# Kernel tuning notes

Measured on AMD Instinct MI355X. Metric: run time of the kernel, lower is better.

The kernel has to match this reference:

```python
import jax, jax.numpy as jnp
import numpy as np

N, E, V_IN, HID, U_IN, B, MEM = 50000, 800000, 128, 128, 64, 64, 128
CAT = V_IN + HID + U_IN  # 320 == hidden*2 + u_in
ALPHA = 0.5
EPS = 1e-5


def setup_inputs() -> dict:
    key = jax.random.key(0)
    ks = jax.random.split(key, 12)
    x = jax.random.normal(ks[0], (N, V_IN), dtype=jnp.float32)
    edge_index = jax.random.randint(ks[1], (2, E), 0, N, dtype=jnp.int64)
    edge_attr = jax.random.normal(ks[2], (E, HID), dtype=jnp.float32)
    u = jax.random.normal(ks[3], (B, U_IN), dtype=jnp.float32)
    batch = jnp.sort(jax.random.randint(ks[4], (N,), 0, B, dtype=jnp.int64))
    Mk = jax.random.normal(ks[5], (MEM, CAT), dtype=jnp.float32)
    Mv = jax.random.normal(ks[6], (MEM, CAT), dtype=jnp.float32)
    ln_gamma = jnp.ones((CAT,), dtype=jnp.float32)
    ln_beta = jnp.zeros((CAT,), dtype=jnp.float32)
    W1 = jax.random.normal(ks[7], (CAT, HID), dtype=jnp.float32) * (1.0 / np.sqrt(CAT))
    b1 = jnp.zeros((HID,), dtype=jnp.float32)
    W2 = jax.random.normal(ks[8], (HID, HID), dtype=jnp.float32) * (1.0 / np.sqrt(HID))
    b2 = jnp.zeros((HID,), dtype=jnp.float32)
    return {"x": x, "edge_index": edge_index, "edge_attr": edge_attr, "u": u,
            "batch": batch, "Mk": Mk, "Mv": Mv, "ln_gamma": ln_gamma,
            "ln_beta": ln_beta, "W1": W1, "b1": b1, "W2": W2, "b2": b2}


def reference(x, edge_index, edge_attr, u, batch, Mk, Mv, ln_gamma, ln_beta, W1, b1, W2, b2):
    # scatter_add over destination nodes
    agg = jax.ops.segment_sum(edge_attr, edge_index[1], num_segments=N)  # [N, HID]
    out = jnp.concatenate([x, agg, u[batch]], axis=1)  # [N, CAT]
    # LayerNorm over last dim
    mu = jnp.mean(out, axis=-1, keepdims=True)
    var = jnp.var(out, axis=-1, keepdims=True)
    out = (out - mu) * jax.lax.rsqrt(var + EPS) * ln_gamma + ln_beta
    # External attention: [N,CAT] @ [CAT,MEM] -> softmax over MEM -> @ [MEM,CAT]
    scores = jnp.einsum('nc,mc->nm', out, Mk)
    attn = jax.nn.softmax(scores, axis=-1)
    attn_out = jnp.einsum('nm,mc->nc', attn, Mv)
    out = ALPHA * attn_out + (1.0 - ALPHA) * out
    # MLP
    h = jax.nn.relu(out @ W1 + b1)
    return h @ W2 + b2
```

## Files before the change

### kernel.cpp

```cpp
#include <hip/hip_runtime.h>

#define NN   50000
#define EE   800000
#define VIN  128
#define HIDN 128
#define UIN  64
#define MEMN 128
#define CATN 320
#define LN_EPS 1e-5f
#define SCAN_NB 196

typedef __attribute__((ext_vector_type(8))) short short8;
typedef __attribute__((ext_vector_type(4))) float f32x4;
typedef __attribute__((ext_vector_type(4))) unsigned int uint4v;
typedef __attribute__((ext_vector_type(4))) unsigned short ushort4v;
typedef unsigned short ushort_t;

__device__ inline ushort_t f32_bf16(float f) {
    unsigned u = __float_as_uint(f);
    return (ushort_t)((u + 0x7FFFu + ((u >> 16) & 1u)) >> 16);
}
__device__ inline float bf16_f32(ushort_t h) {
    return __uint_as_float(((unsigned)h) << 16);
}
__device__ inline unsigned pack_hl(float y) {
    unsigned u  = __float_as_uint(y);
    unsigned hi = (u + 0x7FFFu + ((u >> 16) & 1u)) & 0xFFFF0000u;
    float    lo = y - __uint_as_float(hi);
    unsigned v  = __float_as_uint(lo);
    unsigned l16 = ((v + 0x7FFFu + ((v >> 16) & 1u)) >> 16) & 0xFFFFu;
    return hi | l16;
}

__global__ void hist_kernel(const int* __restrict__ edge_dst, int* __restrict__ count)
{
    int gid = blockIdx.x * 256 + threadIdx.x;
    if (gid < EE) atomicAdd(&count[edge_dst[gid]], 1);
}

__global__ void block_sum_kernel(const int* __restrict__ count, int* __restrict__ partials)
{
    __shared__ int s[256];
    const int tid = threadIdx.x;
    const int gid = blockIdx.x * 256 + tid;
    s[tid] = (gid < NN) ? count[gid] : 0;
    __syncthreads();
    for (int off = 128; off >= 1; off >>= 1) {
        if (tid < off) s[tid] += s[tid + off];
        __syncthreads();
    }
    if (tid == 0) partials[blockIdx.x] = s[0];
}

__global__ void scan_partials_kernel(int* __restrict__ partials)
{
    __shared__ int s[256];
    const int tid = threadIdx.x;
    const int v = (tid < SCAN_NB) ? partials[tid] : 0;
    s[tid] = v;
    __syncthreads();
    for (int off = 1; off < 256; off <<= 1) {
        int t = (tid >= off) ? s[tid - off] : 0;
        __syncthreads();
        s[tid] += t;
        __syncthreads();
    }
    if (tid < SCAN_NB) partials[tid] = s[tid] - v;
}

__global__ void make_offsets_kernel(const int* __restrict__ count,
                                    const int* __restrict__ partials,
                                    int* __restrict__ offsets)
{
    __shared__ int s[256];
    const int tid = threadIdx.x;
    const int gid = blockIdx.x * 256 + tid;
    const int v = (gid < NN) ? count[gid] : 0;
    s[tid] = v;
    __syncthreads();
    for (int off = 1; off < 256; off <<= 1) {
        int t = (tid >= off) ? s[tid - off] : 0;
        __syncthreads();
        s[tid] += t;
        __syncthreads();
    }
    if (gid < NN) offsets[gid] = partials[blockIdx.x] + s[tid] - v;
}

__global__ void fill_kernel(const int* __restrict__ edge_dst,
                            const int* __restrict__ offsets,
                            int* __restrict__ cursor,
                            int* __restrict__ bucket)
{
    int gid = blockIdx.x * 256 + threadIdx.x;
    if (gid >= EE) return;
    const int d = edge_dst[gid];
    const int p = atomicAdd(&cursor[d], 1);
    bucket[offsets[d] + p] = gid;
}

__global__ void prep_all_kernel(const float* __restrict__ Mk,
                                const float* __restrict__ Mv,
                                const float* __restrict__ W1,
                                const float* __restrict__ W2,
                                ushort_t* __restrict__ mk_hi,
                                ushort_t* __restrict__ mk_lo,
                                ushort_t* __restrict__ mv_t,
                                ushort_t* __restrict__ w1_t,
                                ushort_t* __restrict__ w2_t)
{
    int i = blockIdx.x * 256 + threadIdx.x;
    if (i < MEMN * CATN) {
        const float f = Mk[i];
        const ushort_t h = f32_bf16(f);
        mk_hi[i] = h;
        mk_lo[i] = f32_bf16(f - bf16_f32(h));
    }
    if (i < CATN * MEMN) {
        const int c = i >> 7, m = i & 127;
        mv_t[i] = f32_bf16(Mv[m * CATN + c]);
    }
    if (i < HIDN * CATN) {
        const int n = i / CATN, k = i - n * CATN;
        w1_t[i] = f32_bf16(W1[k * HIDN + n]);
    }
    if (i < HIDN * HIDN) {
        const int n = i >> 7, k = i & 127;
        w2_t[i] = f32_bf16(W2[k * HIDN + n]);
    }
}

__global__ __launch_bounds__(256) void gather_ln_kernel(
    const float* __restrict__ edge_attr,
    const int*   __restrict__ bucket,
    const int*   __restrict__ offsets,
    const int*   __restrict__ count,
    const float* __restrict__ x,
    const float* __restrict__ u,
    const int*   __restrict__ batch,
    const float* __restrict__ gamma,
    const float* __restrict__ beta,
    unsigned*    __restrict__ ln_pk)
{
    const int wid  = (blockIdx.x * 256 + threadIdx.x) >> 6;
    const int lane = threadIdx.x & 63;
    if (wid >= NN) return;

    const int start = offsets[wid];
    const int deg   = count[wid];
    const float2* ea2 = reinterpret_cast<const float2*>(edge_attr);
    float2 a = make_float2(0.f, 0.f);
    int i = 0;
    const int d4 = deg & ~3;
    for (; i < d4; i += 4) {
        const int e0 = bucket[start + i];
        const int e1 = bucket[start + i + 1];
        const int e2 = bucket[start + i + 2];
        const int e3 = bucket[start + i + 3];
        const float2 v0 = ea2[(size_t)e0 * 64 + lane];
        const float2 v1 = ea2[(size_t)e1 * 64 + lane];
        const float2 v2 = ea2[(size_t)e2 * 64 + lane];
        const float2 v3 = ea2[(size_t)e3 * 64 + lane];
        a.x += (v0.x + v1.x) + (v2.x + v3.x);
        a.y += (v0.y + v1.y) + (v2.y + v3.y);
    }
    for (; i < deg; ++i) {
        const int e = bucket[start + i];
        const float2 v = ea2[(size_t)e * 64 + lane];
        a.x += v.x;
        a.y += v.y;
    }
    const float2 xv = reinterpret_cast<const float2*>(x)[(size_t)wid * 64 + lane];
    const float  uv = u[batch[wid] * UIN + lane];

    float s = xv.x + xv.y + a.x + a.y + uv;
    float q = xv.x * xv.x + xv.y * xv.y + a.x * a.x + a.y * a.y + uv * uv;
    #pragma unroll
    for (int off = 32; off >= 1; off >>= 1) {
        s += __shfl_xor(s, off);
        q += __shfl_xor(q, off);
    }
    const float mu  = s * (1.0f / CATN);
    const float var = q * (1.0f / CATN) - mu * mu;
    const float rs  = rsqrtf(var + LN_EPS);

    const float2 g0 = reinterpret_cast<const float2*>(gamma)[lane];
    const float2 g1 = reinterpret_cast<const float2*>(gamma)[64 + lane];
    const float  g2 = gamma[256 + lane];
    const float2 t0 = reinterpret_cast<const float2*>(beta)[lane];
    const float2 t1 = reinterpret_cast<const float2*>(beta)[64 + lane];
    const float  t2 = beta[256 + lane];

    unsigned* row = ln_pk + (size_t)wid * CATN;
    uint2 p01, p23;
    p01.x = pack_hl((xv.x - mu) * rs * g0.x + t0.x);
    p01.y = pack_hl((xv.y - mu) * rs * g0.y + t0.y);
    p23.x = pack_hl((a.x - mu) * rs * g1.x + t1.x);
    p23.y = pack_hl((a.y - mu) * rs * g1.y + t1.y);
    reinterpret_cast<uint2*>(row)[lane]       = p01;
    reinterpret_cast<uint2*>(row + 128)[lane] = p23;
    row[256 + lane] = pack_hl((uv - mu) * rs * g2 + t2);
}

#define MSTR 328
#define PSTR 136

__global__ __launch_bounds__(512) void node_mfma_kernel(
    const unsigned* __restrict__ ln_pk,
    const ushort_t* __restrict__ mk_hi,
    const ushort_t* __restrict__ mk_lo,
    const ushort_t* __restrict__ mv_t,
    const ushort_t* __restrict__ w1_t,
    const ushort_t* __restrict__ w2_t,
    const float*    __restrict__ b1,
    const float*    __restrict__ b2,
    float*          __restrict__ out)
{
    __shared__ __align__(16) ushort_t s_lnh[32 * MSTR];
    __shared__ __align__(16) ushort_t s_lnl[32 * MSTR];
    __shared__ __align__(16) ushort_t s_P[32 * PSTR];
    __shared__ __align__(16) float2   s_part[16 * 16];

    const int tid  = threadIdx.x;
    const int wv   = tid >> 6;
    const int lane = tid & 63;
    const int l15  = lane & 15;
    const int l4   = lane >> 4;
    const int node0 = blockIdx.x * 32;

    const f32x4 zero4 = {0.f, 0.f, 0.f, 0.f};

    for (int j = tid; j < 32 * 80; j += 512) {
        const int nl = j / 80;
        const int c0 = (j - nl * 80) * 4;
        int ng = node0 + nl; ng = (ng < NN) ? ng : (NN - 1);
        const uint4v p = *(const uint4v*)(ln_pk + (size_t)ng * CATN + c0);
        ushort4v h4, l4v;
        h4.x = (ushort_t)(p.x >> 16);  l4v.x = (ushort_t)(p.x & 0xFFFFu);
        h4.y = (ushort_t)(p.y >> 16);  l4v.y = (ushort_t)(p.y & 0xFFFFu);
        h4.z = (ushort_t)(p.z >> 16);  l4v.z = (ushort_t)(p.z & 0xFFFFu);
        h4.w = (ushort_t)(p.w >> 16);  l4v.w = (ushort_t)(p.w & 0xFFFFu);
        *(ushort4v*)(s_lnh + nl * MSTR + c0) = h4;
        *(ushort4v*)(s_lnl + nl * MSTR + c0) = l4v;
    }
    __syncthreads();

    {
        f32x4 acc[2];
        acc[0] = zero4; acc[1] = zero4;

        #pragma unroll 2
        for (int kc = 0; kc < 10; ++kc) {
            const int koff = kc * 32 + l4 * 8;
            const int mr = wv * 16 + l15;
            short8 amh = *(const short8*)(mk_hi + (size_t)mr * CATN + koff);
            short8 aml = *(const short8*)(mk_lo + (size_t)mr * CATN + koff);
            short8 bnh[2], bnl[2];
            #pragma unroll
            for (int bt = 0; bt < 2; ++bt) {
                bnh[bt] = *(const short8*)(s_lnh + (bt * 16 + l15) * MSTR + koff);
                bnl[bt] = *(const short8*)(s_lnl + (bt * 16 + l15) * MSTR + koff);
            }
            #pragma unroll
            for (int bt = 0; bt < 2; ++bt) {
                acc[bt] = __builtin_amdgcn_mfma_f32_16x16x32_bf16(amh, bnh[bt], acc[bt], 0, 0, 0);
                acc[bt] = __builtin_amdgcn_mfma_f32_16x16x32_bf16(aml, bnh[bt], acc[bt], 0, 0, 0);
                acc[bt] = __builtin_amdgcn_mfma_f32_16x16x32_bf16(amh, bnl[bt], acc[bt], 0, 0, 0);
            }
        }

        #pragma unroll
        for (int bt = 0; bt < 2; ++bt) {
            float mx = acc[bt][0];
            #pragma unroll
            for (int r = 1; r < 4; ++r) mx = fmaxf(mx, acc[bt][r]);
            mx = fmaxf(mx, __shfl_xor(mx, 16));
            mx = fmaxf(mx, __shfl_xor(mx, 32));
            float sm = 0.f;
            #pragma unroll
            for (int r = 0; r < 4; ++r) sm += __expf(acc[bt][r] - mx);
            sm += __shfl_xor(sm, 16);
            sm += __shfl_xor(sm, 32);
            if (l4 == 0) s_part[(wv * 2 + bt) * 16 + l15] = make_float2(mx, sm);
        }
        __syncthreads();
        #pragma unroll
        for (int bt = 0; bt < 2; ++bt) {
            float mg = -1e30f;
            float2 pw[8];
            #pragma unroll
            for (int w = 0; w < 8; ++w) {
                pw[w] = s_part[(w * 2 + bt) * 16 + l15];
                mg = fmaxf(mg, pw[w].x);
            }
            float sg = 0.f;
            #pragma unroll
            for (int w = 0; w < 8; ++w) sg += pw[w].y * __expf(pw[w].x - mg);
            const float inv = 1.f / sg;
            ushort_t* prow = s_P + (bt * 16 + l15) * PSTR + wv * 16 + l4 * 4;
            #pragma unroll
            for (int r = 0; r < 4; ++r)
                prow[r] = f32_bf16(__expf(acc[bt][r] - mg) * inv);
        }
    }
    __syncthreads();

    {
        const int mt = wv & 1;
        const int cg = wv >> 1;
        f32x4 acc[5];
        #pragma unroll
        for (int nn = 0; nn < 5; ++nn) acc[nn] = zero4;

        #pragma unroll
        for (int kc = 0; kc < 4; ++kc) {
            const int koff = kc * 32 + l4 * 8;
            short8 ap = *(const short8*)(s_P + (mt * 16 + l15) * PSTR + koff);
            short8 bv[5];
            #pragma unroll
            for (int nn = 0; nn < 5; ++nn) {
                const int c = (cg * 5 + nn) * 16 + l15;
                bv[nn] = *(const short8*)(mv_t + (size_t)c * MEMN + koff);
            }
            #pragma unroll
            for (int nn = 0; nn < 5; ++nn)
                acc[nn] = __builtin_amdgcn_mfma_f32_16x16x32_bf16(ap, bv[nn], acc[nn], 0, 0, 0);
        }
        __syncthreads();
        #pragma unroll
        for (int nn = 0; nn < 5; ++nn)
            #pragma unroll
            for (int r = 0; r < 4; ++r) {
                const int node_l = mt * 16 + l4 * 4 + r;
                const int c = (cg * 5 + nn) * 16 + l15;
                const int idx = node_l * MSTR + c;
                const float lnv = bf16_f32(s_lnh[idx]) + bf16_f32(s_lnl[idx]);
                s_lnh[idx] = f32_bf16(0.5f * (acc[nn][r] + lnv));
            }
    }
    __syncthreads();

    {
        const int mt  = wv & 1;
        const int ng2 = wv >> 1;
        f32x4 acc[2];
        acc[0] = zero4; acc[1] = zero4;

        #pragma unroll 2
        for (int kc = 0; kc < 10; ++kc) {
            const int koff = kc * 32 + l4 * 8;
            short8 am = *(const short8*)(s_lnh + (mt * 16 + l15) * MSTR + koff);
            short8 bw[2];
            #pragma unroll
            for (int nt = 0; nt < 2; ++nt) {
                const int n = (ng2 * 2 + nt) * 16 + l15;
                bw[nt] = *(const short8*)(w1_t + (size_t)n * CATN + koff);
            }
            #pragma unroll
            for (int nt = 0; nt < 2; ++nt)
                acc[nt] = __builtin_amdgcn_mfma_f32_16x16x32_bf16(am, bw[nt], acc[nt], 0, 0, 0);
        }
        float bb[2];
        #pragma unroll
        for (int nt = 0; nt < 2; ++nt) bb[nt] = b1[(ng2 * 2 + nt) * 16 + l15];
        __syncthreads();
        #pragma unroll
        for (int nt = 0; nt < 2; ++nt)
            #pragma unroll
            for (int r = 0; r < 4; ++r) {
                const int node_l = mt * 16 + l4 * 4 + r;
                const int col = (ng2 * 2 + nt) * 16 + l15;
                s_P[node_l * PSTR + col] = f32_bf16(fmaxf(acc[nt][r] + bb[nt], 0.f));
            }
    }
    __syncthreads();

    {
        const int mt  = wv & 1;
        const int ng2 = wv >> 1;
        f32x4 acc[2];
        acc[0] = zero4; acc[1] = zero4;

        #pragma unroll
        for (int kc = 0; kc < 4; ++kc) {
            const int koff = kc * 32 + l4 * 8;
            short8 ah = *(const short8*)(s_P + (mt * 16 + l15) * PSTR + koff);
            short8 bw[2];
            #pragma unroll
            for (int nt = 0; nt < 2; ++nt) {
                const int n = (ng2 * 2 + nt) * 16 + l15;
                bw[nt] = *(const short8*)(w2_t + (size_t)n * HIDN + koff);
            }
            #pragma unroll
            for (int nt = 0; nt < 2; ++nt)
                acc[nt] = __builtin_amdgcn_mfma_f32_16x16x32_bf16(ah, bw[nt], acc[nt], 0, 0, 0);
        }
        float bb[2];
        #pragma unroll
        for (int nt = 0; nt < 2; ++nt) bb[nt] = b2[(ng2 * 2 + nt) * 16 + l15];
        #pragma unroll
        for (int nt = 0; nt < 2; ++nt)
            #pragma unroll
            for (int r = 0; r < 4; ++r) {
                const int ng = node0 + (wv & 1) * 16 + l4 * 4 + r;
                if (ng < NN) {
                    const int col = (ng2 * 2 + nt) * 16 + l15;
                    out[(size_t)ng * HIDN + col] = acc[nt][r] + bb[nt];
                }
            }
    }
}

extern "C" void kernel_launch(void* const* d_in, const int* in_sizes, int n_in,
                              void* d_out, int out_size, void* d_ws, size_t ws_size,
                              hipStream_t stream)
{
    const float* x         = (const float*)d_in[0];
    const int*   edge_idx  = (const int*)  d_in[1];
    const float* edge_attr = (const float*)d_in[2];
    const float* u         = (const float*)d_in[3];
    const int*   batch     = (const int*)  d_in[4];
    const float* Mk        = (const float*)d_in[5];
    const float* Mv        = (const float*)d_in[6];
    const float* gamma     = (const float*)d_in[7];
    const float* beta      = (const float*)d_in[8];
    const float* W1        = (const float*)d_in[9];
    const float* b1        = (const float*)d_in[10];
    const float* W2        = (const float*)d_in[11];
    const float* b2        = (const float*)d_in[12];
    float*       out       = (float*)d_out;

    char* w = (char*)d_ws;
    int*   count     = (int*)w;        w += (size_t)NN * sizeof(int);
    int*   cursor    = (int*)w;        w += (size_t)NN * sizeof(int);
    int*   offsets   = (int*)w;        w += (size_t)NN * sizeof(int);
    int*   partials  = (int*)w;        w += 256 * sizeof(int);
    int*   bucket    = (int*)w;        w += (size_t)EE * sizeof(int);
    w = (char*)(((size_t)w + 255) & ~(size_t)255);
    unsigned* ln_pk  = (unsigned*)w;   w += (size_t)NN * CATN * sizeof(unsigned);
    ushort_t* mk_hi  = (ushort_t*)w;   w += (size_t)MEMN * CATN * 2;
    ushort_t* mk_lo  = (ushort_t*)w;   w += (size_t)MEMN * CATN * 2;
    ushort_t* mv_t   = (ushort_t*)w;   w += (size_t)CATN * MEMN * 2;
    ushort_t* w1_t   = (ushort_t*)w;   w += (size_t)HIDN * CATN * 2;
    ushort_t* w2_t   = (ushort_t*)w;   w += (size_t)HIDN * HIDN * 2;

    const int* edge_dst = edge_idx + EE;

    hipMemsetAsync(count, 0, (size_t)2 * NN * sizeof(int), stream);

    const int eb = (EE + 255) / 256;
    hist_kernel<<<eb, 256, 0, stream>>>(edge_dst, count);
    block_sum_kernel<<<SCAN_NB, 256, 0, stream>>>(count, partials);
    scan_partials_kernel<<<1, 256, 0, stream>>>(partials);
    make_offsets_kernel<<<SCAN_NB, 256, 0, stream>>>(count, partials, offsets);
    fill_kernel<<<eb, 256, 0, stream>>>(edge_dst, offsets, cursor, bucket);

    prep_all_kernel<<<(HIDN * CATN + 255) / 256, 256, 0, stream>>>(
        Mk, Mv, W1, W2, mk_hi, mk_lo, mv_t, w1_t, w2_t);

    gather_ln_kernel<<<(NN * 64 + 255) / 256, 256, 0, stream>>>(
        edge_attr, bucket, offsets, count, x, u, batch, gamma, beta, ln_pk);

    node_mfma_kernel<<<(NN + 31) / 32, 512, 0, stream>>>(
        ln_pk, mk_hi, mk_lo, mv_t, w1_t, w2_t, b1, b2, out);
}
```

Baseline: 324.0 us.

## Shrink node MFMA tile to 16 nodes per 4-wave block; deepen gather unroll

The fused attention/MLP kernel now handles 16 nodes per 256-thread block instead of 32 nodes per 512 threads. Each wave now covers two memory-key tiles and more output columns per node tile, and the cross-wave softmax reduction spans 4 partials instead of 8. This halves shared memory per block, which should raise occupancy and the number of blocks in flight, at the cost of reloading the weight matrices from global memory twice as often per node. The gather kernel also issues the x, u, gamma and beta loads before the edge loop and unrolls edge accumulation by 8 to get more memory requests in flight.

```diff
diff --git a/kernel.cpp b/kernel.cpp
--- a/kernel.cpp
+++ b/kernel.cpp
@@ -146,11 +146,41 @@
     const int lane = threadIdx.x & 63;
     if (wid >= NN) return;
 
+    const float2 xv = reinterpret_cast<const float2*>(x)[(size_t)wid * 64 + lane];
+    const float  uv = u[batch[wid] * UIN + lane];
+    const float2 g0 = reinterpret_cast<const float2*>(gamma)[lane];
+    const float2 g1 = reinterpret_cast<const float2*>(gamma)[64 + lane];
+    const float  g2 = gamma[256 + lane];
+    const float2 t0 = reinterpret_cast<const float2*>(beta)[lane];
+    const float2 t1 = reinterpret_cast<const float2*>(beta)[64 + lane];
+    const float  t2 = beta[256 + lane];
+
     const int start = offsets[wid];
     const int deg   = count[wid];
     const float2* ea2 = reinterpret_cast<const float2*>(edge_attr);
     float2 a = make_float2(0.f, 0.f);
     int i = 0;
+    const int d8 = deg & ~7;
+    for (; i < d8; i += 8) {
+        const int e0 = bucket[start + i];
+        const int e1 = bucket[start + i + 1];
+        const int e2 = bucket[start + i + 2];
+        const int e3 = bucket[start + i + 3];
+        const int e4 = bucket[start + i + 4];
+        const int e5 = bucket[start + i + 5];
+        const int e6 = bucket[start + i + 6];
+        const int e7 = bucket[start + i + 7];
+        const float2 v0 = ea2[(size_t)e0 * 64 + lane];
+        const float2 v1 = ea2[(size_t)e1 * 64 + lane];
+        const float2 v2 = ea2[(size_t)e2 * 64 + lane];
+        const float2 v3 = ea2[(size_t)e3 * 64 + lane];
+        const float2 v4 = ea2[(size_t)e4 * 64 + lane];
+        const float2 v5 = ea2[(size_t)e5 * 64 + lane];
+        const float2 v6 = ea2[(size_t)e6 * 64 + lane];
+        const float2 v7 = ea2[(size_t)e7 * 64 + lane];
+        a.x += ((v0.x + v1.x) + (v2.x + v3.x)) + ((v4.x + v5.x) + (v6.x + v7.x));
+        a.y += ((v0.y + v1.y) + (v2.y + v3.y)) + ((v4.y + v5.y) + (v6.y + v7.y));
+    }
     const int d4 = deg & ~3;
     for (; i < d4; i += 4) {
         const int e0 = bucket[start + i];
@@ -170,8 +200,6 @@
         a.x += v.x;
         a.y += v.y;
     }
-    const float2 xv = reinterpret_cast<const float2*>(x)[(size_t)wid * 64 + lane];
-    const float  uv = u[batch[wid] * UIN + lane];
 
     float s = xv.x + xv.y + a.x + a.y + uv;
     float q = xv.x * xv.x + xv.y * xv.y + a.x * a.x + a.y * a.y + uv * uv;
@@ -183,13 +211,6 @@
     const float mu  = s * (1.0f / CATN);
     const float var = q * (1.0f / CATN) - mu * mu;
     const float rs  = rsqrtf(var + LN_EPS);
-
-    const float2 g0 = reinterpret_cast<const float2*>(gamma)[lane];
-    const float2 g1 = reinterpret_cast<const float2*>(gamma)[64 + lane];
-    const float  g2 = gamma[256 + lane];
-    const float2 t0 = reinterpret_cast<const float2*>(beta)[lane];
-    const float2 t1 = reinterpret_cast<const float2*>(beta)[64 + lane];
-    const float  t2 = beta[256 + lane];
 
     unsigned* row = ln_pk + (size_t)wid * CATN;
     uint2 p01, p23;
@@ -205,7 +226,7 @@
 #define MSTR 328
 #define PSTR 136
 
-__global__ __launch_bounds__(512) void node_mfma_kernel(
+__global__ __launch_bounds__(256) void node_mfma_kernel(
     const unsigned* __restrict__ ln_pk,
     const ushort_t* __restrict__ mk_hi,
     const ushort_t* __restrict__ mk_lo,
@@ -216,24 +237,24 @@
     const float*    __restrict__ b2,
     float*          __restrict__ out)
 {
-    __shared__ __align__(16) ushort_t s_lnh[32 * MSTR];
-    __shared__ __align__(16) ushort_t s_lnl[32 * MSTR];
-    __shared__ __align__(16) ushort_t s_P[32 * PSTR];
-    __shared__ __align__(16) float2   s_part[16 * 16];
+    __shared__ __align__(16) ushort_t s_lnh[16 * MSTR];
+    __shared__ __align__(16) ushort_t s_lnl[16 * MSTR];
+    __shared__ __align__(16) ushort_t s_P[16 * PSTR];
+    __shared__ __align__(16) float2   s_part[4 * 16];
 
     const int tid  = threadIdx.x;
     const int wv   = tid >> 6;
     const int lane = tid & 63;
     const int l15  = lane & 15;
     const int l4   = lane >> 4;
-    const int node0 = blockIdx.x * 32;
+    const int node0 = blockIdx.x * 16;
 
     const f32x4 zero4 = {0.f, 0.f, 0.f, 0.f};
 
-    for (int j = tid; j < 32 * 80; j += 512) {
+    for (int j = tid; j < 16 * 80; j += 256) {
         const int nl = j / 80;
         const int c0 = (j - nl * 80) * 4;
-        int ng = node0 + nl; ng = (ng < NN) ? ng : (NN - 1);
+        const int ng = node0 + nl;
         const uint4v p = *(const uint4v*)(ln_pk + (size_t)ng * CATN + c0);
         ushort4v h4, l4v;
         h4.x = (ushort_t)(p.x >> 16);  l4v.x = (ushort_t)(p.x & 0xFFFFu);
@@ -252,62 +273,58 @@
         #pragma unroll 2
         for (int kc = 0; kc < 10; ++kc) {
             const int koff = kc * 32 + l4 * 8;
-            const int mr = wv * 16 + l15;
-            short8 amh = *(const short8*)(mk_hi + (size_t)mr * CATN + koff);
-            short8 aml = *(const short8*)(mk_lo + (size_t)mr * CATN + koff);
-            short8 bnh[2], bnl[2];
-            #pragma unroll
-            for (int bt = 0; bt < 2; ++bt) {
-                bnh[bt] = *(const short8*)(s_lnh + (bt * 16 + l15) * MSTR + koff);
-                bnl[bt] = *(const short8*)(s_lnl + (bt * 16 + l15) * MSTR + koff);
-            }
-            #pragma unroll
-            for (int bt = 0; bt < 2; ++bt) {
-                acc[bt] = __builtin_amdgcn_mfma_f32_16x16x32_bf16(amh, bnh[bt], acc[bt], 0, 0, 0);
-                acc[bt] = __builtin_amdgcn_mfma_f32_16x16x32_bf16(aml, bnh[bt], acc[bt], 0, 0, 0);
-                acc[bt] = __builtin_amdgcn_mfma_f32_16x16x32_bf16(amh, bnl[bt], acc[bt], 0, 0, 0);
+            short8 amh[2], aml[2];
+            #pragma unroll
+            for (int ai = 0; ai < 2; ++ai) {
+                const int mr = (wv * 2 + ai) * 16 + l15;
+                amh[ai] = *(const short8*)(mk_hi + (size_t)mr * CATN + koff);
+                aml[ai] = *(const short8*)(mk_lo + (size_t)mr * CATN + koff);
+            }
+            const short8 bnh = *(const short8*)(s_lnh + l15 * MSTR + koff);
+            const short8 bnl = *(const short8*)(s_lnl + l15 * MSTR + koff);
+            #pragma unroll
+            for (int ai = 0; ai < 2; ++ai) {
+                acc[ai] = __builtin_amdgcn_mfma_f32_16x16x32_bf16(amh[ai], bnh, acc[ai], 0, 0, 0);
+                acc[ai] = __builtin_amdgcn_mfma_f32_16x16x32_bf16(aml[ai], bnh, acc[ai], 0, 0, 0);
+                acc[ai] = __builtin_amdgcn_mfma_f32_16x16x32_bf16(amh[ai], bnl, acc[ai], 0, 0, 0);
             }
         }
 
-        #pragma unroll
-        for (int bt = 0; bt < 2; ++bt) {
-            float mx = acc[bt][0];
-            #pragma unroll
-            for (int r = 1; r < 4; ++r) mx = fmaxf(mx, acc[bt][r]);
-            mx = fmaxf(mx, __shfl_xor(mx, 16));
-            mx = fmaxf(mx, __shfl_xor(mx, 32));
-            float sm = 0.f;
-            #pragma unroll
-            for (int r = 0; r < 4; ++r) sm += __expf(acc[bt][r] - mx);
-            sm += __shfl_xor(sm, 16);
-            sm += __shfl_xor(sm, 32);
-            if (l4 == 0) s_part[(wv * 2 + bt) * 16 + l15] = make_float2(mx, sm);
-        }
-        __syncthreads();
-        #pragma unroll
-        for (int bt = 0; bt < 2; ++bt) {
-            float mg = -1e30f;
-            float2 pw[8];
-            #pragma unroll
-            for (int w = 0; w < 8; ++w) {
-                pw[w] = s_part[(w * 2 + bt) * 16 + l15];
-                mg = fmaxf(mg, pw[w].x);
-            }
-            float sg = 0.f;
-            #pragma unroll
-            for (int w = 0; w < 8; ++w) sg += pw[w].y * __expf(pw[w].x - mg);
-            const float inv = 1.f / sg;
-            ushort_t* prow = s_P + (bt * 16 + l15) * PSTR + wv * 16 + l4 * 4;
+        float mx = acc[0][0];
+        #pragma unroll
+        for (int ai = 0; ai < 2; ++ai)
+            #pragma unroll
+            for (int r = 0; r < 4; ++r) mx = fmaxf(mx, acc[ai][r]);
+        mx = fmaxf(mx, __shfl_xor(mx, 16));
+        mx = fmaxf(mx, __shfl_xor(mx, 32));
+        float sm = 0.f;
+        #pragma unroll
+        for (int ai = 0; ai < 2; ++ai)
+            #pragma unroll
+            for (int r = 0; r < 4; ++r) sm += __expf(acc[ai][r] - mx);
+        sm += __shfl_xor(sm, 16);
+        sm += __shfl_xor(sm, 32);
+        if (l4 == 0) s_part[wv * 16 + l15] = make_float2(mx, sm);
+        __syncthreads();
+
+        const float2 p0 = s_part[0 * 16 + l15];
+        const float2 p1 = s_part[1 * 16 + l15];
+        const float2 p2 = s_part[2 * 16 + l15];
+        const float2 p3 = s_part[3 * 16 + l15];
+        const float mg = fmaxf(fmaxf(p0.x, p1.x), fmaxf(p2.x, p3.x));
+        const float sg = p0.y * __expf(p0.x - mg) + p1.y * __expf(p1.x - mg)
+                       + p2.y * __expf(p2.x - mg) + p3.y * __expf(p3.x - mg);
+        const float inv = 1.f / sg;
+        ushort_t* prow = s_P + l15 * PSTR + (wv * 2) * 16 + l4 * 4;
+        #pragma unroll
+        for (int ai = 0; ai < 2; ++ai)
             #pragma unroll
             for (int r = 0; r < 4; ++r)
-                prow[r] = f32_bf16(__expf(acc[bt][r] - mg) * inv);
-        }
+                prow[ai * 16 + r] = f32_bf16(__expf(acc[ai][r] - mg) * inv);
     }
     __syncthreads();
 
     {
-        const int mt = wv & 1;
-        const int cg = wv >> 1;
         f32x4 acc[5];
         #pragma unroll
         for (int nn = 0; nn < 5; ++nn) acc[nn] = zero4;
@@ -315,24 +332,23 @@
         #pragma unroll
         for (int kc = 0; kc < 4; ++kc) {
             const int koff = kc * 32 + l4 * 8;
-            short8 ap = *(const short8*)(s_P + (mt * 16 + l15) * PSTR + koff);
+            const short8 ap = *(const short8*)(s_P + l15 * PSTR + koff);
             short8 bv[5];
             #pragma unroll
             for (int nn = 0; nn < 5; ++nn) {
-                const int c = (cg * 5 + nn) * 16 + l15;
+                const int c = (wv * 5 + nn) * 16 + l15;
                 bv[nn] = *(const short8*)(mv_t + (size_t)c * MEMN + koff);
             }
             #pragma unroll
             for (int nn = 0; nn < 5; ++nn)
                 acc[nn] = __builtin_amdgcn_mfma_f32_16x16x32_bf16(ap, bv[nn], acc[nn], 0, 0, 0);
         }
-        __syncthreads();
         #pragma unroll
         for (int nn = 0; nn < 5; ++nn)
             #pragma unroll
             for (int r = 0; r < 4; ++r) {
-                const int node_l = mt * 16 + l4 * 4 + r;
-                const int c = (cg * 5 + nn) * 16 + l15;
+                const int node_l = l4 * 4 + r;
+                const int c = (wv * 5 + nn) * 16 + l15;
                 const int idx = node_l * MSTR + c;
                 const float lnv = bf16_f32(s_lnh[idx]) + bf16_f32(s_lnl[idx]);
                 s_lnh[idx] = f32_bf16(0.5f * (acc[nn][r] + lnv));
@@ -341,19 +357,17 @@
     __syncthreads();
 
     {
-        const int mt  = wv & 1;
-        const int ng2 = wv >> 1;
         f32x4 acc[2];
         acc[0] = zero4; acc[1] = zero4;
 
         #pragma unroll 2
         for (int kc = 0; kc < 10; ++kc) {
             const int koff = kc * 32 + l4 * 8;
-            short8 am = *(const short8*)(s_lnh + (mt * 16 + l15) * MSTR + koff);
+            const short8 am = *(const short8*)(s_lnh + l15 * MSTR + koff);
             short8 bw[2];
             #pragma unroll
             for (int nt = 0; nt < 2; ++nt) {
-                const int n = (ng2 * 2 + nt) * 16 + l15;
+                const int n = (wv * 2 + nt) * 16 + l15;
                 bw[nt] = *(const short8*)(w1_t + (size_t)n * CATN + koff);
             }
             #pragma unroll
@@ -362,33 +376,31 @@
         }
         float bb[2];
         #pragma unroll
-        for (int nt = 0; nt < 2; ++nt) bb[nt] = b1[(ng2 * 2 + nt) * 16 + l15];
+        for (int nt = 0; nt < 2; ++nt) bb[nt] = b1[(wv * 2 + nt) * 16 + l15];
         __syncthreads();
         #pragma unroll
         for (int nt = 0; nt < 2; ++nt)
             #pragma unroll
             for (int r = 0; r < 4; ++r) {
-                const int node_l = mt * 16 + l4 * 4 + r;
-                const int col = (ng2 * 2 + nt) * 16 + l15;
+                const int node_l = l4 * 4 + r;
+                const int col = (wv * 2 + nt) * 16 + l15;
                 s_P[node_l * PSTR + col] = f32_bf16(fmaxf(acc[nt][r] + bb[nt], 0.f));
             }
     }
     __syncthreads();
 
     {
-        const int mt  = wv & 1;
-        const int ng2 = wv >> 1;
         f32x4 acc[2];
         acc[0] = zero4; acc[1] = zero4;
 
         #pragma unroll
         for (int kc = 0; kc < 4; ++kc) {
             const int koff = kc * 32 + l4 * 8;
-            short8 ah = *(const short8*)(s_P + (mt * 16 + l15) * PSTR + koff);
+            const short8 ah = *(const short8*)(s_P + l15 * PSTR + koff);
             short8 bw[2];
             #pragma unroll
             for (int nt = 0; nt < 2; ++nt) {
-                const int n = (ng2 * 2 + nt) * 16 + l15;
+                const int n = (wv * 2 + nt) * 16 + l15;
                 bw[nt] = *(const short8*)(w2_t + (size_t)n * HIDN + koff);
             }
             #pragma unroll
@@ -397,14 +409,14 @@
         }
         float bb[2];
         #pragma unroll
-        for (int nt = 0; nt < 2; ++nt) bb[nt] = b2[(ng2 * 2 + nt) * 16 + l15];
+        for (int nt = 0; nt < 2; ++nt) bb[nt] = b2[(wv * 2 + nt) * 16 + l15];
         #pragma unroll
         for (int nt = 0; nt < 2; ++nt)
             #pragma unroll
             for (int r = 0; r < 4; ++r) {
-                const int ng = node0 + (wv & 1) * 16 + l4 * 4 + r;
+                const int ng = node0 + l4 * 4 + r;
                 if (ng < NN) {
-                    const int col = (ng2 * 2 + nt) * 16 + l15;
+                    const int col = (wv * 2 + nt) * 16 + l15;
                     out[(size_t)ng * HIDN + col] = acc[nt][r] + bb[nt];
                 }
             }
@@ -461,6 +473,6 @@
     gather_ln_kernel<<<(NN * 64 + 255) / 256, 256, 0, stream>>>(
         edge_attr, bucket, offsets, count, x, u, batch, gamma, beta, ln_pk);
 
-    node_mfma_kernel<<<(NN + 31) / 32, 512, 0, stream>>>(
+    node_mfma_kernel<<<NN / 16, 256, 0, stream>>>(
         ln_pk, mk_hi, mk_lo, mv_t, w1_t, w2_t, b1, b2, out);
 }
```

After: 340.5 us. 1.05x slower.
